# Kernel optimization log

Hardware: AMD Instinct MI355X
Metric: run time of the kernel (lower is better)

Reference implementation:

```python
import jax, jax.numpy as jnp
import numpy as np

NQ = 8
DIM = 2 ** NQ  # 256
B = 131072
N_FEAT = NQ + NQ * (NQ - 1) // 2  # 36


def _z_feature_matrix():
    # qubit 0 is the most-significant bit of the basis-state index (outermost kron factor)
    bits = (np.arange(DIM)[:, None] >> np.arange(NQ - 1, -1, -1)[None, :]) & 1
    z = (1.0 - 2.0 * bits).astype(np.float32)  # (DIM, NQ), entries +/-1
    cols = [z[:, i] for i in range(NQ)]  # single-qubit <Z_i>
    for i in range(NQ):
        for j in range(i + 1, NQ):
            cols.append(z[:, i] * z[:, j])  # two-body <Z_i Z_j>
    return jnp.asarray(np.stack(cols, axis=1))  # (DIM, N_FEAT)

S = _z_feature_matrix()


def setup_inputs() -> dict:
    key = jax.random.key(0)
    kx, kw, kb = jax.random.split(key, 3)
    x = jax.random.uniform(kx, (B, NQ), dtype=jnp.float32, minval=0.0, maxval=float(np.pi))
    W = jax.random.normal(kw, (2, N_FEAT), dtype=jnp.float32) / np.sqrt(np.float32(N_FEAT))
    b = jax.random.normal(kb, (2,), dtype=jnp.float32) * 0.01
    return {"x": x, "W": W, "b": b}


def _quantum_features(x):
    bsz = x.shape[0]
    # RY(theta)|0> = cos(theta/2)|0> + sin(theta/2)|1>  (real amplitudes)
    half = 0.5 * x
    amps = jnp.stack([jnp.cos(half), jnp.sin(half)], axis=-1)  # (B, NQ, 2)
    # build batched product statevector via successive outer products
    psi = amps[:, 0]
    for q in range(1, NQ):
        psi = (psi[:, :, None] * amps[:, q][:, None, :]).reshape(bsz, -1)
    # CNOT chain: control i, target i+1 (basis permutation: flip target where control=1)
    for i in range(NQ - 1):
        pre, post = 2 ** i, 2 ** (NQ - i - 2)
        psi = psi.reshape(bsz, pre, 2, 2, post)
        psi = jnp.concatenate(
            [psi[:, :, 0][:, :, None], psi[:, :, 1, ::-1, :][:, :, None]], axis=2
        ).reshape(bsz, DIM)
    probs = psi * psi  # state is real, |psi|^2
    # all 36 Pauli-Z expectations in one GEMM: (B, DIM) @ (DIM, 36)
    return probs @ S


def reference(x, W, b):
    feats = _quantum_features(x)  # (B, 36)
    return feats @ W.T + b  # (B, 2)
```

## Files before the change

kernel.cpp:

```cpp
#include <hip/hip_runtime.h>


#define NQ 8
#define NFEAT 36

__global__ __launch_bounds__(256) void quantum_parity_kernel(
    const float* __restrict__ x,
    const float* __restrict__ W,
    const float* __restrict__ bias,
    float* __restrict__ out,
    int B) {
  int b = blockIdx.x * blockDim.x + threadIdx.x;
  if (b >= B) return;

  const float4* xv = (const float4*)(x + (size_t)b * NQ);
  float4 a0 = xv[0];
  float4 a1 = xv[1];

  float c[NQ];
  c[0] = cosf(a0.x);
  c[1] = cosf(a0.y);
  c[2] = cosf(a0.z);
  c[3] = cosf(a0.w);
  c[4] = cosf(a1.x);
  c[5] = cosf(a1.y);
  c[6] = cosf(a1.z);
  c[7] = cosf(a1.w);

  float F[NFEAT];
  float p = 1.0f;
#pragma unroll
  for (int j = 0; j < NQ; ++j) {
    p *= c[j];
    F[j] = p;
  }
  int k = NQ;
#pragma unroll
  for (int i = 0; i < NQ; ++i) {
    float r = 1.0f;
#pragma unroll
    for (int j = i + 1; j < NQ; ++j) {
      r *= c[j];
      F[k++] = r;
    }
  }

  float y0 = bias[0];
  float y1 = bias[1];
#pragma unroll
  for (int t = 0; t < NFEAT; ++t) {
    y0 = fmaf(W[t], F[t], y0);
    y1 = fmaf(W[NFEAT + t], F[t], y1);
  }

  ((float2*)out)[b] = make_float2(y0, y1);
}

extern "C" void kernel_launch(void* const* d_in, const int* in_sizes, int n_in,
                              void* d_out, int out_size, void* d_ws, size_t ws_size,
                              hipStream_t stream) {
  const float* x = (const float*)d_in[0];
  const float* W = (const float*)d_in[1];
  const float* bias = (const float*)d_in[2];
  float* out = (float*)d_out;

  int B = in_sizes[0] / NQ;
  int block = 256;
  int grid = (B + block - 1) / block;
  quantum_parity_kernel<<<grid, block, 0, stream>>>(x, W, bias, out, B);
}
```

Measured before the change: 58.93 us.

## Use hardware cosine intrinsic and process two samples per thread

Replaces the accurate cosf with the native v_cos_f32 instruction, pre-scaling the input by 1/(2π), which removes the range-reduction software path. Each thread now handles two samples, so the output is written as a single float4 and the weight loads are shared across both samples. This lowers accuracy because the hardware cosine is less precise, and any odd batch size would leave its last sample unprocessed. The kernel is memory-bound at 4 MB read, so the gain depends on how much the cosf cost was hiding.

```diff
diff --git a/kernel.cpp b/kernel.cpp
--- a/kernel.cpp
+++ b/kernel.cpp
@@ -3,29 +3,20 @@
 
 #define NQ 8
 #define NFEAT 36
+#define INV_2PI 0.15915494309189535f
 
-__global__ __launch_bounds__(256) void quantum_parity_kernel(
-    const float* __restrict__ x,
-    const float* __restrict__ W,
-    const float* __restrict__ bias,
-    float* __restrict__ out,
-    int B) {
-  int b = blockIdx.x * blockDim.x + threadIdx.x;
-  if (b >= B) return;
-
-  const float4* xv = (const float4*)(x + (size_t)b * NQ);
-  float4 a0 = xv[0];
-  float4 a1 = xv[1];
-
+__device__ __forceinline__ float2 sample_out(float4 a0, float4 a1,
+                                             const float* __restrict__ W,
+                                             float b0, float b1) {
   float c[NQ];
-  c[0] = cosf(a0.x);
-  c[1] = cosf(a0.y);
-  c[2] = cosf(a0.z);
-  c[3] = cosf(a0.w);
-  c[4] = cosf(a1.x);
-  c[5] = cosf(a1.y);
-  c[6] = cosf(a1.z);
-  c[7] = cosf(a1.w);
+  c[0] = __builtin_amdgcn_cosf(a0.x * INV_2PI);
+  c[1] = __builtin_amdgcn_cosf(a0.y * INV_2PI);
+  c[2] = __builtin_amdgcn_cosf(a0.z * INV_2PI);
+  c[3] = __builtin_amdgcn_cosf(a0.w * INV_2PI);
+  c[4] = __builtin_amdgcn_cosf(a1.x * INV_2PI);
+  c[5] = __builtin_amdgcn_cosf(a1.y * INV_2PI);
+  c[6] = __builtin_amdgcn_cosf(a1.z * INV_2PI);
+  c[7] = __builtin_amdgcn_cosf(a1.w * INV_2PI);
 
   float F[NFEAT];
   float p = 1.0f;
@@ -45,15 +36,35 @@
     }
   }
 
-  float y0 = bias[0];
-  float y1 = bias[1];
+  float y0 = b0, y1 = b1;
 #pragma unroll
   for (int t = 0; t < NFEAT; ++t) {
     y0 = fmaf(W[t], F[t], y0);
     y1 = fmaf(W[NFEAT + t], F[t], y1);
   }
+  return make_float2(y0, y1);
+}
 
-  ((float2*)out)[b] = make_float2(y0, y1);
+__global__ __launch_bounds__(256) void quantum_parity_kernel(
+    const float4* __restrict__ x4,
+    const float* __restrict__ W,
+    const float* __restrict__ bias,
+    float4* __restrict__ out4,
+    int Bhalf) {
+  int t = blockIdx.x * blockDim.x + threadIdx.x;
+  if (t >= Bhalf) return;
+
+  float b0 = bias[0], b1 = bias[1];
+
+  float4 a0 = x4[4 * t + 0];
+  float4 a1 = x4[4 * t + 1];
+  float4 a2 = x4[4 * t + 2];
+  float4 a3 = x4[4 * t + 3];
+
+  float2 r0 = sample_out(a0, a1, W, b0, b1);
+  float2 r1 = sample_out(a2, a3, W, b0, b1);
+
+  out4[t] = make_float4(r0.x, r0.y, r1.x, r1.y);
 }
 
 extern "C" void kernel_launch(void* const* d_in, const int* in_sizes, int n_in,
@@ -65,7 +76,9 @@
   float* out = (float*)d_out;
 
   int B = in_sizes[0] / NQ;
+  int Bhalf = B / 2;
   int block = 256;
-  int grid = (B + block - 1) / block;
-  quantum_parity_kernel<<<grid, block, 0, stream>>>(x, W, bias, out, B);
+  int grid = (Bhalf + block - 1) / block;
+  quantum_parity_kernel<<<grid, block, 0, stream>>>(
+      (const float4*)x, W, bias, (float4*)out, Bhalf);
 }
```

Measured after the change: 58.33 us. No clear change (-1.0%).
